# Performance work log

Measured on AMD Instinct MI355X. Metric: run time of the kernel, lower is better.

Reference implementation:

```python
import jax, jax.numpy as jnp
import numpy as np

N_HEAD = 16

def setup_inputs() -> dict:
    key = jax.random.key(0)
    ks = jax.random.split(key, 6)
    C = 1024
    B, T, Tp = 8, 1024, 64
    s = 0.02
    return {
        "x": jax.random.normal(ks[0], (B, T, C), jnp.float32),
        "prefix_embd": jax.random.normal(ks[1], (B, Tp, C), jnp.float32),
        "w_attn": jax.random.normal(ks[2], (C, 3 * C), jnp.float32) * s,
        "b_attn": jnp.zeros((3 * C,), jnp.float32),
        "w_prefix": jax.random.normal(ks[3], (C, 3 * C), jnp.float32) * s,
        "b_prefix": jnp.zeros((3 * C,), jnp.float32),
        "w_proj": jax.random.normal(ks[4], (C, C), jnp.float32) * s,
        "b_proj": jnp.zeros((C,), jnp.float32),
    }

def _heads(t, H):
    B, T, C = t.shape
    return t.reshape(B, T, H, C // H).transpose(0, 2, 1, 3)  # (B,H,T,d)

def reference(x, prefix_embd, w_attn, b_attn, w_prefix, b_prefix, w_proj, b_proj):
    B, T, C = x.shape
    H = N_HEAD
    d = C // H
    Tp = prefix_embd.shape[1]
    scale = 1.0 / jnp.sqrt(jnp.asarray(d, x.dtype))

    qkv = x @ w_attn + b_attn
    q, k, v = (_heads(t, H) for t in jnp.split(qkv, 3, axis=2))  # (B,H,T,d)

    pqkv = prefix_embd @ w_prefix + b_prefix
    _, k_p, v_p = (_heads(t, H) for t in jnp.split(pqkv, 3, axis=2))  # (B,H,Tp,d)

    causal = jnp.tril(jnp.ones((T, T), bool))  # bias buffer slice
    neg_inf = jnp.asarray(float("-inf"), x.dtype)

    att = jnp.einsum("bhqd,bhkd->bhqk", q, k) * scale
    att = jnp.where(causal[None, None], att, neg_inf)
    att = jax.nn.softmax(att, axis=-1)

    att_p = jnp.einsum("bhqd,bhkd->bhqk", q, k_p) * scale
    att_p = jnp.where(causal[:, :Tp][None, None], att_p, neg_inf)
    att_p = jax.nn.softmax(att_p, axis=-1)

    y = jnp.einsum("bhqk,bhkd->bhqd", att_p, v_p) + jnp.einsum("bhqk,bhkd->bhqd", att, v)
    y = y.transpose(0, 2, 1, 3).reshape(B, T, C)
    return y @ w_proj + b_proj
```

## Files before the change

### kernel.cpp

```cpp
#include <hip/hip_runtime.h>
#include <hip/hip_bf16.h>
#include <cstdint>
#include <cstddef>

typedef __bf16 bf16_t;
typedef bf16_t bf16x8 __attribute__((ext_vector_type(8)));
typedef bf16_t bf16x4 __attribute__((ext_vector_type(4)));
typedef float f32x4 __attribute__((ext_vector_type(4)));

#define NB 8
#define NT 1024
#define NC 1024
#define NH 16
#define ND 64
#define NTP 64

__global__ __launch_bounds__(256) void k_cast_bf16(const float* __restrict__ src,
                                                   bf16_t* __restrict__ dst, int n4) {
    int i = blockIdx.x * 256 + threadIdx.x;
    if (i < n4) {
        float4 f = ((const float4*)src)[i];
        bf16x4 o;
        o[0] = (bf16_t)f.x; o[1] = (bf16_t)f.y; o[2] = (bf16_t)f.z; o[3] = (bf16_t)f.w;
        ((bf16x4*)dst)[i] = o;
    }
}

__global__ __launch_bounds__(256) void k_transpose_cast(const float* __restrict__ src,
                                                        bf16_t* __restrict__ dst,
                                                        int K, int N) {
    __shared__ float tile[32][33];
    int nt = blockIdx.x, kt = blockIdx.y;
    int tx = threadIdx.x & 31;
    int ty = threadIdx.x >> 5;
#pragma unroll
    for (int i = 0; i < 4; i++) {
        int r = ty + i * 8;
        tile[r][tx] = src[(size_t)(kt * 32 + r) * N + nt * 32 + tx];
    }
    __syncthreads();
#pragma unroll
    for (int i = 0; i < 4; i++) {
        int r = ty + i * 8;
        dst[(size_t)(nt * 32 + r) * K + kt * 32 + tx] = (bf16_t)tile[tx][r];
    }
}

__global__ __launch_bounds__(256) void k_vT(const bf16_t* __restrict__ src,
                                            bf16_t* __restrict__ dst, int T) {
    __shared__ bf16_t tile[32][33];
    const int bh = blockIdx.z;
    const int b = bh >> 4, h = bh & 15;
    const int t0 = blockIdx.x * 32, d0 = blockIdx.y * 32;
    const int tx = threadIdx.x & 31;
    const int ty = threadIdx.x >> 5;
#pragma unroll
    for (int i = 0; i < 4; i++) {
        int r = ty + i * 8;
        tile[r][tx] = src[(size_t)(b * T + t0 + r) * 3072 + 2 * NC + h * 64 + d0 + tx];
    }
    __syncthreads();
    const size_t tileBase = ((size_t)bh * (T / 64) + (t0 >> 6)) * 64 * 64;
#pragma unroll
    for (int i = 0; i < 4; i++) {
        int r = ty + i * 8;
        dst[tileBase + (size_t)(d0 + r) * 64 + (t0 & 63) + tx] = tile[tx][r];
    }
}

template <bool OUT_F32>
__global__ __launch_bounds__(256) void k_gemm_bt(const bf16_t* __restrict__ A,
                                                 const bf16_t* __restrict__ BT,
                                                 const float* __restrict__ bias,
                                                 void* __restrict__ Cout,
                                                 int M, int N, int K) {
    __shared__ bf16_t As[128 * 72];
    __shared__ bf16_t Bs[128 * 72];
    const int tid = threadIdx.x;
    const int lane = tid & 63;
    const int wave = tid >> 6;
    const int quad = lane >> 4;
    const int l15 = lane & 15;
    const int wm = (wave >> 1) * 64;
    const int wn = (wave & 1) * 64;
    const size_t rowA0 = (size_t)blockIdx.y * 128;
    const size_t colB0 = (size_t)blockIdx.x * 128;

    const f32x4 fz = {0.f, 0.f, 0.f, 0.f};
    f32x4 acc[4][4];
#pragma unroll
    for (int i = 0; i < 4; i++)
#pragma unroll
        for (int j = 0; j < 4; j++) acc[i][j] = fz;

    for (int k0 = 0; k0 < K; k0 += 64) {
        __syncthreads();
#pragma unroll
        for (int i = 0; i < 4; i++) {
            int c = tid + i * 256;
            int r = c >> 3;
            int kc = (c & 7) * 8;
            uint4 av = *(const uint4*)(A + (rowA0 + r) * K + k0 + kc);
            *(uint4*)(&As[r * 72 + kc]) = av;
            uint4 bv = *(const uint4*)(BT + (colB0 + r) * K + k0 + kc);
            *(uint4*)(&Bs[r * 72 + kc]) = bv;
        }
        __syncthreads();
#pragma unroll
        for (int kk = 0; kk < 2; kk++) {
            bf16x8 af[4], bfr[4];
#pragma unroll
            for (int i = 0; i < 4; i++)
                af[i] = *(const bf16x8*)(&As[(wm + i * 16 + l15) * 72 + kk * 32 + quad * 8]);
#pragma unroll
            for (int j = 0; j < 4; j++)
                bfr[j] = *(const bf16x8*)(&Bs[(wn + j * 16 + l15) * 72 + kk * 32 + quad * 8]);
#pragma unroll
            for (int i = 0; i < 4; i++)
#pragma unroll
                for (int j = 0; j < 4; j++)
                    acc[i][j] = __builtin_amdgcn_mfma_f32_16x16x32_bf16(af[i], bfr[j], acc[i][j], 0, 0, 0);
        }
    }
#pragma unroll
    for (int i = 0; i < 4; i++) {
        size_t row = rowA0 + wm + i * 16 + quad * 4;
#pragma unroll
        for (int j = 0; j < 4; j++) {
            int col = (int)colB0 + wn + j * 16 + l15;
            float bv = bias[col];
#pragma unroll
            for (int r = 0; r < 4; r++) {
                float v = acc[i][j][r] + bv;
                if (OUT_F32)
                    ((float*)Cout)[(row + r) * (size_t)N + col] = v;
                else
                    ((bf16_t*)Cout)[(row + r) * (size_t)N + col] = (bf16_t)v;
            }
        }
    }
}


#define LOADREGS(KB, VB)                                                  \
    rk0 = *(const uint4*)((KB) + (size_t)srow * 3072 + scol);             \
    rk1 = *(const uint4*)((KB) + (size_t)(srow + 32) * 3072 + scol);      \
    rv0 = *(const uint4*)((VB) + (size_t)tid * 8);                        \
    rv1 = *(const uint4*)((VB) + (size_t)(tid + 256) * 8);

#define STAGE(KS, VS)                                     \
    *(uint4*)(&(KS)[srow * 72 + scol]) = rk0;             \
    *(uint4*)(&(KS)[(srow + 32) * 72 + scol]) = rk1;      \
    *(uint4*)(&(VS)[srow * 72 + scol]) = rv0;             \
    *(uint4*)(&(VS)[(srow + 32) * 72 + scol]) = rv1;

#define QK(KS, Sj, j)                                                                  \
    Sj = __builtin_amdgcn_mfma_f32_16x16x32_bf16(                                      \
        aq0, *(const bf16x8*)(&(KS)[((j) * 16 + l15) * 72 + quad * 8]), Sj, 0, 0, 0);  \
    Sj = __builtin_amdgcn_mfma_f32_16x16x32_bf16(                                      \
        aq1, *(const bf16x8*)(&(KS)[((j) * 16 + l15) * 72 + 32 + quad * 8]), Sj, 0, 0, 0);

#define EXPJ(Sj, j, DIAG, LACC)                                         \
    {                                                                   \
        const int n_ = (j) * 16 + l15;                                  \
        _Pragma("unroll") for (int r_ = 0; r_ < 4; r_++) {              \
            float p_ = __expf(Sj[r_] * scale);                          \
            if ((DIAG) && n_ > wave * 16 + quad * 4 + r_) p_ = 0.f;     \
            Sj[r_] = p_;                                                \
            LACC[r_] += p_;                                             \
        }                                                               \
    }

#define PSTORE(Sj, j)                                                   \
    _Pragma("unroll") for (int r_ = 0; r_ < 4; r_++)                    \
        P[(quad * 4 + r_) * 72 + (j) * 16 + l15] = (bf16_t)Sj[r_];

#define PV(VS, Oj, j)                                                                  \
    Oj = __builtin_amdgcn_mfma_f32_16x16x32_bf16(                                      \
        ap0, *(const bf16x8*)(&(VS)[((j) * 16 + l15) * 72 + quad * 8]), Oj, 0, 0, 0);  \
    Oj = __builtin_amdgcn_mfma_f32_16x16x32_bf16(                                      \
        ap1, *(const bf16x8*)(&(VS)[((j) * 16 + l15) * 72 + 32 + quad * 8]), Oj, 0, 0, 0);

#define PROC(KS, VS, DIAG, LACC, O0, O1, O2, O3)                        \
    {                                                                   \
        f32x4 S0 = fz, S1 = fz, S2 = fz, S3 = fz;                       \
        QK(KS, S0, 0) QK(KS, S1, 1) QK(KS, S2, 2) QK(KS, S3, 3)         \
        EXPJ(S0, 0, DIAG, LACC) EXPJ(S1, 1, DIAG, LACC)                 \
        EXPJ(S2, 2, DIAG, LACC) EXPJ(S3, 3, DIAG, LACC)                 \
        PSTORE(S0, 0) PSTORE(S1, 1) PSTORE(S2, 2) PSTORE(S3, 3)         \
        __builtin_amdgcn_s_waitcnt(0xc07f);             \
        __builtin_amdgcn_wave_barrier();                                \
        bf16x8 ap0 = *(const bf16x8*)(&P[l15 * 72 + quad * 8]);         \
        bf16x8 ap1 = *(const bf16x8*)(&P[l15 * 72 + 32 + quad * 8]);    \
        PV(VS, O0, 0) PV(VS, O1, 1) PV(VS, O2, 2) PV(VS, O3, 3)         \
    }

#define STORE_O(Oj, Pj, j)                                                            \
    _Pragma("unroll") for (int r_ = 0; r_ < 4; r_++) {                                \
        float v_ = Oj[r_] * lmv[r_] + Pj[r_] * lpv[r_];                               \
        y[(qrow0 + quad * 4 + r_) * NC + h * 64 + (j) * 16 + l15] = (bf16_t)v_;       \
    }

__global__ __launch_bounds__(256, 2) void k_attn8(const bf16_t* __restrict__ qkv,
                                                  const bf16_t* __restrict__ pqkv,
                                                  const bf16_t* __restrict__ vp,
                                                  const bf16_t* __restrict__ pvp,
                                                  bf16_t* __restrict__ y) {
    const int qt = (NT / 64 - 1) - blockIdx.x;
    const int h = blockIdx.y;
    const int b = blockIdx.z;

    __shared__ bf16_t Ks0[64 * 72], Ks1[64 * 72];
    __shared__ bf16_t Vs0[64 * 72], Vs1[64 * 72];
    __shared__ bf16_t Ps[4][16 * 72];

    const int tid = threadIdx.x;
    const int lane = tid & 63;
    const int wave = tid >> 6;
    const int quad = lane >> 4;
    const int l15 = lane & 15;
    const int srow = tid >> 3;
    const int scol = (tid & 7) * 8;
    const float scale = 0.125f;

    const size_t qrow0 = (size_t)b * NT + (size_t)qt * 64 + wave * 16;
    bf16_t* P = Ps[wave];

    const bf16_t* Kmain = qkv + (size_t)(b * NT) * 3072 + NC + h * 64;
    const bf16_t* Vmain = vp + (size_t)(b * NH + h) * 16 * (64 * 64);

    bf16x8 aq0 = *(const bf16x8*)(qkv + (qrow0 + l15) * 3072 + h * 64 + quad * 8);
    bf16x8 aq1 = *(const bf16x8*)(qkv + (qrow0 + l15) * 3072 + h * 64 + 32 + quad * 8);

    const f32x4 fz = {0.f, 0.f, 0.f, 0.f};
    f32x4 Om0 = fz, Om1 = fz, Om2 = fz, Om3 = fz;
    f32x4 Op0 = fz, Op1 = fz, Op2 = fz, Op3 = fz;
    f32x4 Lm = fz, Lp = fz;
    uint4 rk0, rk1, rv0, rv1;

    LOADREGS(pqkv + (size_t)(b * NTP) * 3072 + NC + h * 64,
             pvp + (size_t)(b * NH + h) * (NTP * 64))
    STAGE(Ks0, Vs0)
    LOADREGS(Kmain, Vmain)
    __syncthreads();
    PROC(Ks0, Vs0, qt == 0, Lp, Op0, Op1, Op2, Op3)
    STAGE(Ks1, Vs1)
    if (qt >= 1) { LOADREGS(Kmain + (size_t)64 * 3072, Vmain + 64 * 64) }

    for (int t = 0; t <= qt; t++) {
        __syncthreads();
        bf16_t* KSc = (t & 1) ? Ks0 : Ks1;
        bf16_t* VSc = (t & 1) ? Vs0 : Vs1;
        if (t < qt) {
            bf16_t* KSn = (t & 1) ? Ks1 : Ks0;
            bf16_t* VSn = (t & 1) ? Vs1 : Vs0;
            STAGE(KSn, VSn)
        }
        if (t + 1 < qt) {
            LOADREGS(Kmain + ((size_t)(t + 2) * 64) * 3072, Vmain + (size_t)(t + 2) * (64 * 64))
        }
        PROC(KSc, VSc, t == qt, Lm, Om0, Om1, Om2, Om3)
    }

    f32x4 lmv, lpv;
#pragma unroll
    for (int r = 0; r < 4; r++) {
        float vm = Lm[r], vpr = Lp[r];
#pragma unroll
        for (int off = 1; off < 16; off <<= 1) {
            vm += __shfl_xor(vm, off, 64);
            vpr += __shfl_xor(vpr, off, 64);
        }
        lmv[r] = 1.0f / vm;
        lpv[r] = 1.0f / vpr;
    }

    STORE_O(Om0, Op0, 0) STORE_O(Om1, Op1, 1) STORE_O(Om2, Op2, 2) STORE_O(Om3, Op3, 3)
}

extern "C" void kernel_launch(void* const* d_in, const int* in_sizes, int n_in,
                              void* d_out, int out_size, void* d_ws, size_t ws_size,
                              hipStream_t stream) {
    (void)in_sizes; (void)n_in; (void)out_size; (void)ws_size;
    const float* x        = (const float*)d_in[0];
    const float* prefix   = (const float*)d_in[1];
    const float* w_attn   = (const float*)d_in[2];
    const float* b_attn   = (const float*)d_in[3];
    const float* w_prefix = (const float*)d_in[4];
    const float* b_prefix = (const float*)d_in[5];
    const float* w_proj   = (const float*)d_in[6];
    const float* b_proj   = (const float*)d_in[7];
    float* out = (float*)d_out;

    char* p = (char*)d_ws;
    auto carve = [&](size_t bytes) {
        char* q = p;
        p += (bytes + 255) & ~(size_t)255;
        return q;
    };
    bf16_t* xb   = (bf16_t*)carve((size_t)NB * NT * NC * 2);
    bf16_t* pb   = (bf16_t*)carve((size_t)NB * NTP * NC * 2);
    bf16_t* wTa  = (bf16_t*)carve((size_t)3 * NC * NC * 2);
    bf16_t* wTp  = (bf16_t*)carve((size_t)3 * NC * NC * 2);
    bf16_t* wTpr = (bf16_t*)carve((size_t)NC * NC * 2);
    bf16_t* qkv  = (bf16_t*)carve((size_t)NB * NT * 3 * NC * 2);
    bf16_t* pqkv = (bf16_t*)carve((size_t)NB * NTP * 3 * NC * 2);
    bf16_t* yb   = (bf16_t*)carve((size_t)NB * NT * NC * 2);

    k_cast_bf16<<<(NB * NT * NC / 4 + 255) / 256, 256, 0, stream>>>(x, xb, NB * NT * NC / 4);
    k_cast_bf16<<<(NB * NTP * NC / 4 + 255) / 256, 256, 0, stream>>>(prefix, pb, NB * NTP * NC / 4);
    k_transpose_cast<<<dim3(3 * NC / 32, NC / 32), 256, 0, stream>>>(w_attn, wTa, NC, 3 * NC);
    k_transpose_cast<<<dim3(3 * NC / 32, NC / 32), 256, 0, stream>>>(w_prefix, wTp, NC, 3 * NC);
    k_transpose_cast<<<dim3(NC / 32, NC / 32), 256, 0, stream>>>(w_proj, wTpr, NC, NC);
    k_gemm_bt<false><<<dim3(3 * NC / 128, NB * NT / 128), 256, 0, stream>>>(
        xb, wTa, b_attn, qkv, NB * NT, 3 * NC, NC);
    k_gemm_bt<false><<<dim3(3 * NC / 128, NB * NTP / 128), 256, 0, stream>>>(
        pb, wTp, b_prefix, pqkv, NB * NTP, 3 * NC, NC);
    bf16_t* vp  = xb;
    bf16_t* pvp = pb;
    k_vT<<<dim3(NT / 32, ND / 32, NB * NH), 256, 0, stream>>>(qkv, vp, NT);
    k_vT<<<dim3(NTP / 32, ND / 32, NB * NH), 256, 0, stream>>>(pqkv, pvp, NTP);
    k_attn8<<<dim3(NT / 64, NH, NB), 256, 0, stream>>>(qkv, pqkv, vp, pvp, yb);
    k_gemm_bt<true><<<dim3(NC / 128, NB * NT / 128), 256, 0, stream>>>(
        yb, wTpr, b_proj, out, NB * NT, NC, NC);
}
```

Baseline: 324.3 us.

## Fuse input bf16 cast and V transpose into QKV GEMM kernels

The QKV and prefix GEMMs now read fp32 activations directly and convert them to bf16 while staging into shared memory, which removes the separate cast kernels. Their epilogues also write the V columns straight into the tiled transposed layout the attention kernel expects, which removes the k_vT kernels. Four launches and the intermediate round trips through memory go away. In exchange, the GEMM A-tile loads read twice as many bytes per tile, since they now fetch fp32 instead of bf16.

```diff
diff --git a/kernel.cpp b/kernel.cpp
--- a/kernel.cpp
+++ b/kernel.cpp
@@ -14,17 +14,6 @@
 #define NH 16
 #define ND 64
 #define NTP 64
-
-__global__ __launch_bounds__(256) void k_cast_bf16(const float* __restrict__ src,
-                                                   bf16_t* __restrict__ dst, int n4) {
-    int i = blockIdx.x * 256 + threadIdx.x;
-    if (i < n4) {
-        float4 f = ((const float4*)src)[i];
-        bf16x4 o;
-        o[0] = (bf16_t)f.x; o[1] = (bf16_t)f.y; o[2] = (bf16_t)f.z; o[3] = (bf16_t)f.w;
-        ((bf16x4*)dst)[i] = o;
-    }
-}
 
 __global__ __launch_bounds__(256) void k_transpose_cast(const float* __restrict__ src,
                                                         bf16_t* __restrict__ dst,
@@ -46,34 +35,13 @@
     }
 }
 
-__global__ __launch_bounds__(256) void k_vT(const bf16_t* __restrict__ src,
-                                            bf16_t* __restrict__ dst, int T) {
-    __shared__ bf16_t tile[32][33];
-    const int bh = blockIdx.z;
-    const int b = bh >> 4, h = bh & 15;
-    const int t0 = blockIdx.x * 32, d0 = blockIdx.y * 32;
-    const int tx = threadIdx.x & 31;
-    const int ty = threadIdx.x >> 5;
-#pragma unroll
-    for (int i = 0; i < 4; i++) {
-        int r = ty + i * 8;
-        tile[r][tx] = src[(size_t)(b * T + t0 + r) * 3072 + 2 * NC + h * 64 + d0 + tx];
-    }
-    __syncthreads();
-    const size_t tileBase = ((size_t)bh * (T / 64) + (t0 >> 6)) * 64 * 64;
-#pragma unroll
-    for (int i = 0; i < 4; i++) {
-        int r = ty + i * 8;
-        dst[tileBase + (size_t)(d0 + r) * 64 + (t0 & 63) + tx] = tile[tx][r];
-    }
-}
-
-template <bool OUT_F32>
-__global__ __launch_bounds__(256) void k_gemm_bt(const bf16_t* __restrict__ A,
-                                                 const bf16_t* __restrict__ BT,
-                                                 const float* __restrict__ bias,
-                                                 void* __restrict__ Cout,
-                                                 int M, int N, int K) {
+template <bool AF32, int OMODE, int TSH>
+__global__ __launch_bounds__(256) void k_gemm_f(const void* __restrict__ A,
+                                                const bf16_t* __restrict__ BT,
+                                                const float* __restrict__ bias,
+                                                void* __restrict__ Cout,
+                                                bf16_t* __restrict__ Vout,
+                                                int M, int N, int K) {
     __shared__ bf16_t As[128 * 72];
     __shared__ bf16_t Bs[128 * 72];
     const int tid = threadIdx.x;
@@ -100,9 +68,21 @@
             int c = tid + i * 256;
             int r = c >> 3;
             int kc = (c & 7) * 8;
-            uint4 av = *(const uint4*)(A + (rowA0 + r) * K + k0 + kc);
-            *(uint4*)(&As[r * 72 + kc]) = av;
-            uint4 bv = *(const uint4*)(BT + (colB0 + r) * K + k0 + kc);
+            if (AF32) {
+                const float* Af = (const float*)A + (rowA0 + r) * (size_t)K + k0 + kc;
+                float4 a0 = *(const float4*)Af;
+                float4 a1 = *(const float4*)(Af + 4);
+                bf16x8 av;
+                av[0] = (bf16_t)a0.x; av[1] = (bf16_t)a0.y;
+                av[2] = (bf16_t)a0.z; av[3] = (bf16_t)a0.w;
+                av[4] = (bf16_t)a1.x; av[5] = (bf16_t)a1.y;
+                av[6] = (bf16_t)a1.z; av[7] = (bf16_t)a1.w;
+                *(bf16x8*)(&As[r * 72 + kc]) = av;
+            } else {
+                uint4 av = *(const uint4*)((const bf16_t*)A + (rowA0 + r) * (size_t)K + k0 + kc);
+                *(uint4*)(&As[r * 72 + kc]) = av;
+            }
+            uint4 bv = *(const uint4*)(BT + (colB0 + r) * (size_t)K + k0 + kc);
             *(uint4*)(&Bs[r * 72 + kc]) = bv;
         }
         __syncthreads();
@@ -122,6 +102,7 @@
                     acc[i][j] = __builtin_amdgcn_mfma_f32_16x16x32_bf16(af[i], bfr[j], acc[i][j], 0, 0, 0);
         }
     }
+    const bool vpath = (OMODE == 2) && (colB0 >= (size_t)(2 * NC));
 #pragma unroll
     for (int i = 0; i < 4; i++) {
         size_t row = rowA0 + wm + i * 16 + quad * 4;
@@ -129,13 +110,26 @@
         for (int j = 0; j < 4; j++) {
             int col = (int)colB0 + wn + j * 16 + l15;
             float bv = bias[col];
-#pragma unroll
-            for (int r = 0; r < 4; r++) {
-                float v = acc[i][j][r] + bv;
-                if (OUT_F32)
-                    ((float*)Cout)[(row + r) * (size_t)N + col] = v;
-                else
-                    ((bf16_t*)Cout)[(row + r) * (size_t)N + col] = (bf16_t)v;
+            if (vpath) {
+                int hh = (col - 2 * NC) >> 6;
+                int dd = col & 63;
+                int bb = (int)(row >> TSH);
+                int tt = (int)row & ((1 << TSH) - 1);
+                size_t addr = ((size_t)(bb * NH + hh) * (1 << (TSH - 6)) + (tt >> 6)) * 4096
+                              + (size_t)dd * 64 + (tt & 63);
+                bf16x4 vv;
+#pragma unroll
+                for (int r = 0; r < 4; r++) vv[r] = (bf16_t)(acc[i][j][r] + bv);
+                *(bf16x4*)(Vout + addr) = vv;
+            } else {
+#pragma unroll
+                for (int r = 0; r < 4; r++) {
+                    float v = acc[i][j][r] + bv;
+                    if (OMODE == 1)
+                        ((float*)Cout)[(row + r) * (size_t)N + col] = v;
+                    else
+                        ((bf16_t*)Cout)[(row + r) * (size_t)N + col] = (bf16_t)v;
+                }
             }
         }
     }
@@ -298,8 +292,8 @@
         p += (bytes + 255) & ~(size_t)255;
         return q;
     };
-    bf16_t* xb   = (bf16_t*)carve((size_t)NB * NT * NC * 2);
-    bf16_t* pb   = (bf16_t*)carve((size_t)NB * NTP * NC * 2);
+    bf16_t* vp   = (bf16_t*)carve((size_t)NB * NT * NC * 2);
+    bf16_t* pvp  = (bf16_t*)carve((size_t)NB * NTP * NC * 2);
     bf16_t* wTa  = (bf16_t*)carve((size_t)3 * NC * NC * 2);
     bf16_t* wTp  = (bf16_t*)carve((size_t)3 * NC * NC * 2);
     bf16_t* wTpr = (bf16_t*)carve((size_t)NC * NC * 2);
@@ -307,20 +301,14 @@
     bf16_t* pqkv = (bf16_t*)carve((size_t)NB * NTP * 3 * NC * 2);
     bf16_t* yb   = (bf16_t*)carve((size_t)NB * NT * NC * 2);
 
-    k_cast_bf16<<<(NB * NT * NC / 4 + 255) / 256, 256, 0, stream>>>(x, xb, NB * NT * NC / 4);
-    k_cast_bf16<<<(NB * NTP * NC / 4 + 255) / 256, 256, 0, stream>>>(prefix, pb, NB * NTP * NC / 4);
     k_transpose_cast<<<dim3(3 * NC / 32, NC / 32), 256, 0, stream>>>(w_attn, wTa, NC, 3 * NC);
     k_transpose_cast<<<dim3(3 * NC / 32, NC / 32), 256, 0, stream>>>(w_prefix, wTp, NC, 3 * NC);
     k_transpose_cast<<<dim3(NC / 32, NC / 32), 256, 0, stream>>>(w_proj, wTpr, NC, NC);
-    k_gemm_bt<false><<<dim3(3 * NC / 128, NB * NT / 128), 256, 0, stream>>>(
-        xb, wTa, b_attn, qkv, NB * NT, 3 * NC, NC);
-    k_gemm_bt<false><<<dim3(3 * NC / 128, NB * NTP / 128), 256, 0, stream>>>(
-        pb, wTp, b_prefix, pqkv, NB * NTP, 3 * NC, NC);
-    bf16_t* vp  = xb;
-    bf16_t* pvp = pb;
-    k_vT<<<dim3(NT / 32, ND / 32, NB * NH), 256, 0, stream>>>(qkv, vp, NT);
-    k_vT<<<dim3(NTP / 32, ND / 32, NB * NH), 256, 0, stream>>>(pqkv, pvp, NTP);
+    k_gemm_f<true, 2, 10><<<dim3(3 * NC / 128, NB * NT / 128), 256, 0, stream>>>(
+        x, wTa, b_attn, qkv, vp, NB * NT, 3 * NC, NC);
+    k_gemm_f<true, 2, 6><<<dim3(3 * NC / 128, NB * NTP / 128), 256, 0, stream>>>(
+        prefix, wTp, b_prefix, pqkv, pvp, NB * NTP, 3 * NC, NC);
     k_attn8<<<dim3(NT / 64, NH, NB), 256, 0, stream>>>(qkv, pqkv, vp, pvp, yb);
-    k_gemm_bt<true><<<dim3(NC / 128, NB * NT / 128), 256, 0, stream>>>(
-        yb, wTpr, b_proj, out, NB * NT, NC, NC);
+    k_gemm_f<false, 1, 6><<<dim3(NC / 128, NB * NT / 128), 256, 0, stream>>>(
+        yb, wTpr, b_proj, out, nullptr, NB * NT, NC, NC);
 }
```

Result: slower. 358.4 us (+10.5%).
